# Kernel optimization log

Measured on AMD Instinct MI355X. Metric: run time of the kernel, lower is better.

## Reference

```python
import jax, jax.numpy as jnp
import numpy as np
from jax import lax

CORR = 16  # corr_size in the original module


def _adaptive_pool16(x):
    # exact adaptive avg pool when H, W divisible by 16 (torch-equivalent)
    B, C, H, W = x.shape
    return x.reshape(B, C, CORR, H // CORR, CORR, W // CORR).mean(axis=(3, 5))


def _l2_normalize(x, eps=1e-12):
    # torch F.normalize default: L2 over dim=1, norm clamped to eps
    n = jnp.sqrt(jnp.sum(x * x, axis=1, keepdims=True))
    return x / jnp.maximum(n, eps)


def _instance_norm(x, eps=1e-5):
    # InstanceNorm2d, affine=False, biased variance over H,W per (b,c)
    mu = x.mean(axis=(2, 3), keepdims=True)
    var = jnp.mean((x - mu) ** 2, axis=(2, 3), keepdims=True)
    return (x - mu) * lax.rsqrt(var + eps)


def _corr_reduce(x, W1, b1, W2, b2):
    # 1x1 conv (256 -> fc) + bias
    y = jnp.einsum('bchw,oc->bohw', x, W1[:, :, 0, 0]) + b1[None, :, None, None]
    y = jax.nn.relu(_instance_norm(y))
    # 3x3 conv, padding=1, stride=1
    y = lax.conv_general_dilated(y, W2, (1, 1), 'SAME',
                                 dimension_numbers=('NCHW', 'OIHW', 'NCHW'))
    return y + b2[None, :, None, None]


def _corr(feat):
    # pooled [B,C,16,16] used as per-sample bank of 256 1x1 conv kernels
    pooled = _adaptive_pool16(feat)                      # [B,C,16,16]
    norm = _l2_normalize(feat)                           # [B,C,H,W]
    B, C = pooled.shape[:2]
    ker = pooled.reshape(B, C, CORR * CORR)              # [B,C,256]
    # corr[b,p,h,w] = sum_c ker[b,c,p] * norm[b,c,h,w]
    return jnp.einsum('bcp,bchw->bphw', ker, norm)


def setup_inputs() -> dict:
    key = jax.random.key(0)
    ks = jax.random.split(key, 6)
    B, C, H, W = 16, 256, 96, 96
    fc = 256
    return {
        'F_infrared': jax.random.normal(ks[0], (B, C, H, W), jnp.float32),
        'F_visible': jax.random.normal(ks[1], (B, C, H, W), jnp.float32),
        'W1': jax.random.normal(ks[2], (fc, CORR * CORR, 1, 1), jnp.float32) * 0.05,
        'b1': jax.random.normal(ks[3], (fc,), jnp.float32) * 0.05,
        'W2': jax.random.normal(ks[4], (fc, fc, 3, 3), jnp.float32) * 0.05,
        'b2': jax.random.normal(ks[5], (fc,), jnp.float32) * 0.05,
    }


def reference(F_infrared, F_visible, W1, b1, W2, b2):
    VIS_corr = _corr_reduce(_corr(F_visible), W1, b1, W2, b2)
    IR_corr = _corr_reduce(_corr(F_infrared), W1, b1, W2, b2)
    return (IR_corr, VIS_corr)
```

## Files before the change

### kernel.cpp

```cpp
#include <hip/hip_runtime.h>
#include <hip/hip_bf16.h>

#define BATCH 16
#define CH    256
#define HH    96
#define WW    96
#define HWSZ  9216
#define FCH   256
#define PP    256

typedef float f32x4 __attribute__((ext_vector_type(4)));
typedef short bf16x8 __attribute__((ext_vector_type(8)));
typedef unsigned short ushortT;

#define APAD_ELEMS 2458624
#define APAD_CHUNKS 307328

__device__ __forceinline__ void gload16(const void* g, void* l) {
    __builtin_amdgcn_global_load_lds((const __attribute__((address_space(1))) void*)g,
                                     (__attribute__((address_space(3))) void*)l, 16, 0, 0);
}
__device__ __forceinline__ float bfu2f(ushortT u) {
    return __uint_as_float(((unsigned)u) << 16);
}
__device__ __forceinline__ ushortT f2bfu(float f) {
    __hip_bfloat16 hb = __float2bfloat16(f);
    return *reinterpret_cast<ushortT*>(&hb);
}

__global__ void fpack_k(const float* __restrict__ feat, ushortT* __restrict__ fpack,
                        float* __restrict__ rnorm)
{
    int b = blockIdx.y;
    int hw = blockIdx.x * 256 + threadIdx.x;
    const float* src = feat + (size_t)b * CH * HWSZ + hw;
    uint4* dst = (uint4*)fpack + (size_t)b * 32 * HWSZ + hw;
    float ss = 0.f;
    for (int cb = 0; cb < 32; ++cb) {
        union { ushortT u[8]; uint4 v; } pk;
#pragma unroll
        for (int i = 0; i < 8; ++i) {
            float v = src[(size_t)(cb * 8 + i) * HWSZ];
            ss += v * v;
            pk.u[i] = f2bfu(v);
        }
        dst[(size_t)cb * HWSZ] = pk.v;
    }
    rnorm[b * HWSZ + hw] = 1.0f / fmaxf(sqrtf(ss), 1e-12f);
}

__global__ void pool16b_k(const ushortT* __restrict__ fpack, float* __restrict__ pooled)
{
    int cb = blockIdx.x, b = blockIdx.y;
    const uint4* fp = (const uint4*)fpack + ((size_t)b * 32 + cb) * HWSZ;
    int t = threadIdx.x;
    int pr = t >> 4, pc = t & 15;
    float s[8] = {};
#pragma unroll
    for (int i = 0; i < 6; ++i) {
#pragma unroll
        for (int j = 0; j < 6; ++j) {
            uint4 v = fp[(pr * 6 + i) * WW + pc * 6 + j];
            const ushortT* u = (const ushortT*)&v;
#pragma unroll
            for (int k = 0; k < 8; ++k) s[k] += bfu2f(u[k]);
        }
    }
#pragma unroll
    for (int k = 0; k < 8; ++k)
        pooled[((size_t)b * CH + cb * 8 + k) * PP + t] = s[k] * (1.0f / 36.0f);
}

__global__ void gemmM_k(const float* __restrict__ W1, const float* __restrict__ pooled,
                        ushortT* __restrict__ Mb16)
{
    int b = blockIdx.z;
    int o0 = blockIdx.y * 16, c0 = blockIdx.x * 16;
    int ty = threadIdx.y, tx = threadIdx.x;
    __shared__ float Ws[16][17], Ps[16][17];
    float acc = 0.f;
    for (int p0 = 0; p0 < PP; p0 += 16) {
        Ws[ty][tx] = W1[(o0 + ty) * PP + p0 + tx];
        Ps[ty][tx] = pooled[((size_t)b * CH + (c0 + ty)) * PP + p0 + tx];
        __syncthreads();
#pragma unroll
        for (int p = 0; p < 16; ++p) acc += Ws[ty][p] * Ps[tx][p];
        __syncthreads();
    }
    int c = c0 + tx, o = o0 + ty;
    Mb16[(((size_t)b * 32 + (c >> 3)) * 256 + o) * 8 + (c & 7)] = f2bfu(acc);
}

__global__ void repack_w2_k(const float* __restrict__ W2, ushortT* __restrict__ W2r2)
{
    int e = blockIdx.x * 256 + threadIdx.x;
    int ci = e & 7, o = (e >> 3) & 255, cb = (e >> 11) & 31, s = e >> 16;
    int c = cb * 8 + ci;
    W2r2[e] = f2bfu(W2[((size_t)o * 256 + c) * 9 + s]);
}

__global__ void zborder_k(uint4* __restrict__ apad)
{
    int bl = blockIdx.x;
    uint4* apC = apad + (size_t)bl * APAD_CHUNKS;
    uint4 z; z.x = 0; z.y = 0; z.z = 0; z.w = 0;
    for (int e = threadIdx.x; e < 3136; e += 256) {
        apC[e] = z;
        apC[(size_t)97 * 32 * 98 + e] = z;
    }
    for (int e = threadIdx.x; e < 3072; e += 256) {
        int row = 1 + (e >> 5), cb = e & 31;
        size_t base = (size_t)(row * 32 + cb) * 98;
        apC[base] = z;
        apC[base + 97] = z;
    }
}

__global__ __launch_bounds__(256, 4) void gemmYm_k(const ushortT* __restrict__ Mb16,
                                                   const ushortT* __restrict__ fpack,
                                                   const float* __restrict__ rnorm,
                                                   ushortT* __restrict__ apad, int b0)
{
    int bl = blockIdx.z, bg = b0 + bl;
    int hw0 = blockIdx.x * 128;
    int o0 = blockIdx.y * 128;
    int tid = threadIdx.x, wave = tid >> 6, lane = tid & 63;
    int wm = wave >> 1, wn = wave & 1;
    int lr = lane & 15, kb = lane >> 4;

    __shared__ __align__(16) char smem[33280];

    const uint4* MbC = (const uint4*)Mb16 + (size_t)bg * 32 * 256;
    const uint4* fpC = (const uint4*)fpack + (size_t)bg * 32 * HWSZ;

    f32x4 acc[4][4] = {};

    auto STAGE = [&](int buf, int s) {
        int cb0 = s * 4;
        uint4* A = (uint4*)smem + (size_t)buf * 1024;
        uint4* B = A + 512;
#pragma unroll
        for (int i = 0; i < 2; ++i) {
            int e = tid + i * 256;
            int kk = e >> 7, j = e & 127;
            gload16(MbC + (size_t)(cb0 + kk) * 256 + o0 + j, A + e);
            gload16(fpC + (size_t)(cb0 + kk) * HWSZ + hw0 + j, B + e);
        }
    };

    STAGE(0, 0);
    for (int s = 0; s < 8; ++s) {
        int buf = s & 1;
        __syncthreads();
        if (s < 7) STAGE(buf ^ 1, s + 1);
        const bf16x8* AsV = (const bf16x8*)(smem + (size_t)buf * 16384);
        const bf16x8* BsV = AsV + 512;
        bf16x8 af[4], bfv[4];
#pragma unroll
        for (int mf = 0; mf < 4; ++mf) af[mf] = AsV[kb * 128 + wm * 64 + mf * 16 + lr];
#pragma unroll
        for (int nf = 0; nf < 4; ++nf) bfv[nf] = BsV[kb * 128 + wn * 64 + nf * 16 + lr];
#pragma unroll
        for (int mf = 0; mf < 4; ++mf)
#pragma unroll
            for (int nf = 0; nf < 4; ++nf)
                acc[mf][nf] = __builtin_amdgcn_mfma_f32_16x16x32_bf16(af[mf], bfv[nf], acc[mf][nf], 0, 0, 0);
    }
    __syncthreads();

    float rn[4];
#pragma unroll
    for (int nf = 0; nf < 4; ++nf)
        rn[nf] = rnorm[(size_t)bg * HWSZ + hw0 + wn * 64 + nf * 16 + lr];

    ushortT* T = (ushortT*)smem;
#pragma unroll
    for (int mf = 0; mf < 4; ++mf)
#pragma unroll
        for (int nf = 0; nf < 4; ++nf)
#pragma unroll
            for (int r = 0; r < 4; ++r)
                T[(wn * 64 + nf * 16 + lr) * 130 + wm * 64 + mf * 16 + kb * 4 + r] =
                    f2bfu(acc[mf][nf][r] * rn[nf]);
    __syncthreads();

    uint4* apC = (uint4*)apad + (size_t)bl * APAD_CHUNKS;
    int ob0 = blockIdx.y * 16;
#pragma unroll
    for (int i = 0; i < 8; ++i) {
        int e = tid + i * 256;
        int hw_l = e >> 4, ob = e & 15;
        uint4 v = *(uint4*)&T[hw_l * 130 + ob * 8];
        int hw = hw0 + hw_l;
        int h = hw / 96, w = hw - h * 96;
        apC[(size_t)((h + 1) * 32 + ob0 + ob) * 98 + (w + 1)] = v;
    }
}

__global__ void instats2_k(const ushortT* __restrict__ apad, float* __restrict__ mu,
                           float* __restrict__ istd)
{
    int ob = blockIdx.x, bl = blockIdx.y;
    const uint4* apC = (const uint4*)apad + (size_t)bl * APAD_CHUNKS;
    float s[8] = {}, s2[8] = {};
    for (int e = threadIdx.x; e < HWSZ; e += 256) {
        int row = e / 96;
        int w = e - row * 96;
        uint4 v = apC[(size_t)((row + 1) * 32 + ob) * 98 + w + 1];
        const ushortT* u = (const ushortT*)&v;
#pragma unroll
        for (int k = 0; k < 8; ++k) {
            float f = bfu2f(u[k]);
            s[k] += f; s2[k] += f * f;
        }
    }
#pragma unroll
    for (int off = 32; off > 0; off >>= 1) {
#pragma unroll
        for (int k = 0; k < 8; ++k) {
            s[k]  += __shfl_down(s[k],  off, 64);
            s2[k] += __shfl_down(s2[k], off, 64);
        }
    }
    __shared__ float sh[4][16];
    int wid = threadIdx.x >> 6;
    if ((threadIdx.x & 63) == 0) {
#pragma unroll
        for (int k = 0; k < 8; ++k) { sh[wid][k] = s[k]; sh[wid][8 + k] = s2[k]; }
    }
    __syncthreads();
    if (threadIdx.x < 8) {
        int k = threadIdx.x;
        float S  = sh[0][k] + sh[1][k] + sh[2][k] + sh[3][k];
        float S2 = sh[0][8 + k] + sh[1][8 + k] + sh[2][8 + k] + sh[3][8 + k];
        float m   = S * (1.0f / HWSZ);
        float var = S2 * (1.0f / HWSZ) - m * m;
        if (var < 0.f) var = 0.f;
        mu[bl * 256 + ob * 8 + k]   = m;
        istd[bl * 256 + ob * 8 + k] = rsqrtf(var + 1e-5f);
    }
}

__global__ void nr_k(ushortT* __restrict__ apad, const float* __restrict__ mu,
                     const float* __restrict__ istd)
{
    int row = blockIdx.x + 1, bl = blockIdx.y;
    __shared__ float smu[256], sis[256];
    smu[threadIdx.x] = mu[bl * 256 + threadIdx.x];
    sis[threadIdx.x] = istd[bl * 256 + threadIdx.x];
    __syncthreads();
    uint4* apC = (uint4*)apad + (size_t)bl * APAD_CHUNKS + (size_t)row * 32 * 98;
    for (int e = threadIdx.x; e < 3072; e += 256) {
        int ob = e / 96;
        int w = e - ob * 96 + 1;
        uint4 v = apC[(size_t)ob * 98 + w];
        ushortT* u = (ushortT*)&v;
#pragma unroll
        for (int k = 0; k < 8; ++k) {
            float f = (bfu2f(u[k]) - smu[ob * 8 + k]) * sis[ob * 8 + k];
            u[k] = f2bfu(f > 0.f ? f : 0.f);
        }
        apC[(size_t)ob * 98 + w] = v;
    }
}

__global__ __launch_bounds__(256, 2) void conv3m3_k(const ushortT* __restrict__ apad,
                                                    const ushortT* __restrict__ W2r2,
                                                    const float* __restrict__ b2,
                                                    float* __restrict__ out)
{
    int h0 = blockIdx.x * 2;
    int o0 = blockIdx.y * 64;
    int bl = blockIdx.z;
    int tid = threadIdx.x;
    int wave = tid >> 6, lane = tid & 63;
    int wr = wave >> 1, wh = wave & 1;
    int lr = lane & 15, kb = lane >> 4;

    __shared__ __align__(16) uint4 AsC[2][768];
    __shared__ __align__(16) uint4 BsC[2][1024];

    const uint4* apadC = (const uint4*)apad + (size_t)bl * APAD_CHUNKS;
    const uint4* w2C   = (const uint4*)W2r2;

    f32x4 acc[4][3] = {};

    auto STAGE = [&](int buf, int it) {
        int kh = it >> 3, cb0 = (it & 7) << 2;
#pragma unroll
        for (int i = 0; i < 3; ++i) {
            int e = tid + i * 256;
            int o = e & 63, kk = (e >> 6) & 3, kw = e >> 8;
            gload16(w2C + (size_t)((kh * 3 + kw) * 32 + cb0 + kk) * 256 + o0 + o,
                    &AsC[buf][e]);
        }
#pragma unroll
        for (int i = 0; i < 4; ++i) {
            int e = tid + i * 256;
            int se = e < 784 ? e : 783;
            int w = se % 98, r = se / 98;
            int rr = r >> 2, kk = r & 3;
            gload16(apadC + (size_t)((h0 + kh + rr) * 32 + cb0 + kk) * 98 + w,
                    &BsC[buf][e]);
        }
    };

    STAGE(0, 0);
    for (int it = 0; it < 24; ++it) {
        int buf = it & 1;
        __syncthreads();
        if (it < 23) STAGE(buf ^ 1, it + 1);
        const bf16x8* AsV = (const bf16x8*)&AsC[buf][0];
        const bf16x8* BsV = (const bf16x8*)&BsC[buf][0];
#pragma unroll
        for (int kw = 0; kw < 3; ++kw) {
            bf16x8 af[4];
#pragma unroll
            for (int mf = 0; mf < 4; ++mf)
                af[mf] = AsV[(kw * 4 + kb) * 64 + mf * 16 + lr];
#pragma unroll
            for (int nf = 0; nf < 3; ++nf) {
                bf16x8 bfr = BsV[(wr * 4 + kb) * 98 + wh * 48 + nf * 16 + lr + kw];
#pragma unroll
                for (int mf = 0; mf < 4; ++mf)
                    acc[mf][nf] = __builtin_amdgcn_mfma_f32_16x16x32_bf16(af[mf], bfr, acc[mf][nf], 0, 0, 0);
            }
        }
    }

    int h = h0 + wr;
    float* obase = out + (size_t)bl * FCH * HWSZ + (size_t)h * WW + wh * 48;
#pragma unroll
    for (int mf = 0; mf < 4; ++mf) {
#pragma unroll
        for (int r = 0; r < 4; ++r) {
            int o = o0 + mf * 16 + kb * 4 + r;
            float bias = b2[o];
            float* orow = obase + (size_t)o * HWSZ;
#pragma unroll
            for (int nf = 0; nf < 3; ++nf)
                orow[nf * 16 + lr] = acc[mf][nf][r] + bias;
        }
    }
}

extern "C" void kernel_launch(void* const* d_in, const int* in_sizes, int n_in,
                              void* d_out, int out_size, void* d_ws, size_t ws_size,
                              hipStream_t stream)
{
    const float* Fir  = (const float*)d_in[0];
    const float* Fvis = (const float*)d_in[1];
    const float* W1   = (const float*)d_in[2];
    const float* W2   = (const float*)d_in[4];
    const float* b2   = (const float*)d_in[5];
    float* out = (float*)d_out;

    char* w = (char*)d_ws;
    const size_t poolB = (size_t)BATCH * CH * PP * 4;
    const size_t MbB   = (size_t)BATCH * 32 * 256 * 8 * 2;
    const size_t rnB   = (size_t)BATCH * HWSZ * 4;
    const size_t stB   = (size_t)BATCH * FCH * 4;
    const size_t w2rB  = (size_t)9 * 32 * 256 * 8 * 2;
    const size_t fpB   = (size_t)BATCH * 32 * HWSZ * 8 * 2;

    size_t off = 0;
    float*   pooled = (float*)(w + off);   off += poolB;
    ushortT* Mb16   = (ushortT*)(w + off); off += MbB;
    float*   rnorm  = (float*)(w + off);   off += rnB;
    float*   mu     = (float*)(w + off);   off += stB;
    float*   istd   = (float*)(w + off);   off += stB;
    ushortT* W2r2   = (ushortT*)(w + off); off += w2rB;
    ushortT* fpack  = (ushortT*)(w + off); off += fpB;
    const size_t fixed = off;

    const size_t apadB = (size_t)APAD_ELEMS * 2;
    size_t avail = ws_size > fixed ? ws_size - fixed : 0;
    int NB = (int)(avail / apadB);
    if (NB > BATCH) NB = BATCH;
    if (NB < 1) NB = 1;
    ushortT* apad = (ushortT*)(w + fixed);

    repack_w2_k<<<2304, 256, 0, stream>>>(W2, W2r2);
    zborder_k<<<NB, 256, 0, stream>>>((uint4*)apad);

    for (int f = 0; f < 2; ++f) {
        const float* feat = (f == 0) ? Fir : Fvis;
        float* o_ = out + (size_t)f * BATCH * FCH * HWSZ;

        fpack_k<<<dim3(36, BATCH), 256, 0, stream>>>(feat, fpack, rnorm);
        pool16b_k<<<dim3(32, BATCH), 256, 0, stream>>>(fpack, pooled);
        gemmM_k<<<dim3(16, 16, BATCH), dim3(16, 16), 0, stream>>>(W1, pooled, Mb16);

        for (int b0 = 0; b0 < BATCH; b0 += NB) {
            int nb = BATCH - b0 < NB ? BATCH - b0 : NB;
            gemmYm_k<<<dim3(72, 2, nb), 256, 0, stream>>>(Mb16, fpack, rnorm, apad, b0);
            instats2_k<<<dim3(32, nb), 256, 0, stream>>>(apad, mu, istd);
            nr_k<<<dim3(96, nb), 256, 0, stream>>>(apad, mu, istd);
            conv3m3_k<<<dim3(48, 4, nb), 256, 0, stream>>>(apad, W2r2, b2,
                                                           o_ + (size_t)b0 * FCH * HWSZ);
        }
    }
}
```

Baseline: 773.8 us.

## Enlarge conv3x3 tile to four rows and stage all taps per channel chunk

The 3x3 conv kernel now computes four output rows per block (one per wave, full 96-wide row) instead of two. Each channel chunk stages all 9 weight taps and the six input rows it needs at once, so neighbouring kh taps share the staged input rows and fewer halo rows are reloaded. The cost is dropping double buffering: loads and MFMA no longer overlap within a block. Shared memory per block rises to about 77 KB and the grid is halved, which may reduce occupancy and latency hiding.

```diff
diff --git a/kernel.cpp b/kernel.cpp
--- a/kernel.cpp
+++ b/kernel.cpp
@@ -264,72 +264,68 @@
     }
 }
 
-__global__ __launch_bounds__(256, 2) void conv3m3_k(const ushortT* __restrict__ apad,
+__global__ __launch_bounds__(256, 2) void conv3m4_k(const ushortT* __restrict__ apad,
                                                     const ushortT* __restrict__ W2r2,
                                                     const float* __restrict__ b2,
                                                     float* __restrict__ out)
 {
-    int h0 = blockIdx.x * 2;
+    int h0 = blockIdx.x * 4;
     int o0 = blockIdx.y * 64;
     int bl = blockIdx.z;
     int tid = threadIdx.x;
     int wave = tid >> 6, lane = tid & 63;
-    int wr = wave >> 1, wh = wave & 1;
     int lr = lane & 15, kb = lane >> 4;
 
-    __shared__ __align__(16) uint4 AsC[2][768];
-    __shared__ __align__(16) uint4 BsC[2][1024];
+    __shared__ __align__(16) uint4 AsC[2304];
+    __shared__ __align__(16) uint4 BsC[2560];
 
     const uint4* apadC = (const uint4*)apad + (size_t)bl * APAD_CHUNKS;
     const uint4* w2C   = (const uint4*)W2r2;
-
-    f32x4 acc[4][3] = {};
-
-    auto STAGE = [&](int buf, int it) {
-        int kh = it >> 3, cb0 = (it & 7) << 2;
-#pragma unroll
-        for (int i = 0; i < 3; ++i) {
+    const bf16x8* AsV = (const bf16x8*)AsC;
+    const bf16x8* BsV = (const bf16x8*)BsC;
+
+    f32x4 acc[4][6] = {};
+
+    for (int ci = 0; ci < 8; ++ci) {
+        int cb0 = ci * 4;
+        __syncthreads();
+#pragma unroll
+        for (int i = 0; i < 9; ++i) {
             int e = tid + i * 256;
-            int o = e & 63, kk = (e >> 6) & 3, kw = e >> 8;
-            gload16(w2C + (size_t)((kh * 3 + kw) * 32 + cb0 + kk) * 256 + o0 + o,
-                    &AsC[buf][e]);
-        }
-#pragma unroll
-        for (int i = 0; i < 4; ++i) {
+            int o = e & 63, kk = (e >> 6) & 3, s = e >> 8;
+            gload16(w2C + (size_t)(s * 32 + cb0 + kk) * 256 + o0 + o, &AsC[e]);
+        }
+#pragma unroll
+        for (int i = 0; i < 10; ++i) {
             int e = tid + i * 256;
-            int se = e < 784 ? e : 783;
+            int se = e < 2352 ? e : e - 256;
             int w = se % 98, r = se / 98;
-            int rr = r >> 2, kk = r & 3;
-            gload16(apadC + (size_t)((h0 + kh + rr) * 32 + cb0 + kk) * 98 + w,
-                    &BsC[buf][e]);
-        }
-    };
-
-    STAGE(0, 0);
-    for (int it = 0; it < 24; ++it) {
-        int buf = it & 1;
-        __syncthreads();
-        if (it < 23) STAGE(buf ^ 1, it + 1);
-        const bf16x8* AsV = (const bf16x8*)&AsC[buf][0];
-        const bf16x8* BsV = (const bf16x8*)&BsC[buf][0];
-#pragma unroll
-        for (int kw = 0; kw < 3; ++kw) {
-            bf16x8 af[4];
-#pragma unroll
-            for (int mf = 0; mf < 4; ++mf)
-                af[mf] = AsV[(kw * 4 + kb) * 64 + mf * 16 + lr];
-#pragma unroll
-            for (int nf = 0; nf < 3; ++nf) {
-                bf16x8 bfr = BsV[(wr * 4 + kb) * 98 + wh * 48 + nf * 16 + lr + kw];
+            int kk = r & 3, row = r >> 2;
+            gload16(apadC + (size_t)((h0 + row) * 32 + cb0 + kk) * 98 + w, &BsC[e]);
+        }
+        __syncthreads();
+#pragma unroll
+        for (int kh = 0; kh < 3; ++kh) {
+#pragma unroll
+            for (int kw = 0; kw < 3; ++kw) {
+                int s = kh * 3 + kw;
+                bf16x8 af[4];
 #pragma unroll
                 for (int mf = 0; mf < 4; ++mf)
-                    acc[mf][nf] = __builtin_amdgcn_mfma_f32_16x16x32_bf16(af[mf], bfr, acc[mf][nf], 0, 0, 0);
+                    af[mf] = AsV[(s * 4 + kb) * 64 + mf * 16 + lr];
+#pragma unroll
+                for (int nf = 0; nf < 6; ++nf) {
+                    bf16x8 bfr = BsV[((wave + kh) * 4 + kb) * 98 + nf * 16 + lr + kw];
+#pragma unroll
+                    for (int mf = 0; mf < 4; ++mf)
+                        acc[mf][nf] = __builtin_amdgcn_mfma_f32_16x16x32_bf16(af[mf], bfr, acc[mf][nf], 0, 0, 0);
+                }
             }
         }
     }
 
-    int h = h0 + wr;
-    float* obase = out + (size_t)bl * FCH * HWSZ + (size_t)h * WW + wh * 48;
+    int h = h0 + wave;
+    float* obase = out + (size_t)bl * FCH * HWSZ + (size_t)h * WW;
 #pragma unroll
     for (int mf = 0; mf < 4; ++mf) {
 #pragma unroll
@@ -338,7 +334,7 @@
             float bias = b2[o];
             float* orow = obase + (size_t)o * HWSZ;
 #pragma unroll
-            for (int nf = 0; nf < 3; ++nf)
+            for (int nf = 0; nf < 6; ++nf)
                 orow[nf * 16 + lr] = acc[mf][nf][r] + bias;
         }
     }
@@ -396,7 +392,7 @@
             gemmYm_k<<<dim3(72, 2, nb), 256, 0, stream>>>(Mb16, fpack, rnorm, apad, b0);
             instats2_k<<<dim3(32, nb), 256, 0, stream>>>(apad, mu, istd);
             nr_k<<<dim3(96, nb), 256, 0, stream>>>(apad, mu, istd);
-            conv3m3_k<<<dim3(48, 4, nb), 256, 0, stream>>>(apad, W2r2, b2,
+            conv3m4_k<<<dim3(24, 4, nb), 256, 0, stream>>>(apad, W2r2, b2,
                                                            o_ + (size_t)b0 * FCH * HWSZ);
         }
     }
```

Result: faster. 637.4 us, median of 2 (-17.6%).
